# Optimization experiments

Measured on AMD Instinct MI355X. Metric: run time of the kernel, lower is better.

## Reference

```python
import jax, jax.numpy as jnp
import numpy as np

K = 16
EPS = 1e-5
SLOPE = 0.2


def knn_idx(k, xyz_k, xyz_q):
    # xyz_k: (B,Nk,3), xyz_q: (B,Nq,3) -> (B,Nq,k) indices of k nearest in xyz_k
    d = (jnp.sum(xyz_q * xyz_q, -1, keepdims=True)
         - 2.0 * jnp.einsum('bqc,bkc->bqk', xyz_q, xyz_k)
         + jnp.sum(xyz_k * xyz_k, -1)[:, None, :])
    _, idx = jax.lax.top_k(-d, k)
    return idx


def graph_feature(coor_q, x_q, coor_k, x_k):
    # coor_*: (B,N*,3); x_q: (B,C,Nq); x_k: (B,C,Nk) -> (B,2C,Nq,K)
    idx = knn_idx(K, coor_k, coor_q)                      # (B,Nq,K)
    nbr = jax.vmap(lambda xk, i: xk[:, i])(x_k, idx)       # (B,C,Nq,K)
    xq = x_q[:, :, :, None]                                # (B,C,Nq,1)
    xq = jnp.broadcast_to(xq, nbr.shape)
    return jnp.concatenate([nbr - xq, xq], axis=1)


def group_norm(x, gamma, beta, groups=4):
    B, C, N, Kk = x.shape
    xg = x.reshape(B, groups, C // groups, N, Kk)
    mu = jnp.mean(xg, axis=(2, 3, 4), keepdims=True)
    var = jnp.var(xg, axis=(2, 3, 4), keepdims=True)
    xn = ((xg - mu) / jnp.sqrt(var + EPS)).reshape(B, C, N, Kk)
    return xn * gamma[None, :, None, None] + beta[None, :, None, None]


def cgl(f, W, gamma, beta):
    # 1x1 Conv2d (no bias) + GroupNorm(4) + LeakyReLU(0.2)
    y = jnp.einsum('oc,bcnk->bonk', W, f)
    return jax.nn.leaky_relu(group_norm(y, gamma, beta), SLOPE)


def fps(xyz, m):
    # furthest point sampling. xyz: (B,N,3) -> (B,m) int32
    B, N, _ = xyz.shape
    first = jnp.zeros((B,), jnp.int32)

    def body(carry, _):
        dist, last = carry
        lp = jnp.take_along_axis(xyz, last[:, None, None].astype(jnp.int32), axis=1)  # (B,1,3)
        d = jnp.sum((xyz - lp) ** 2, -1)
        dist = jnp.minimum(dist, d)
        nxt = jnp.argmax(dist, -1).astype(jnp.int32)
        return (dist, nxt), nxt

    init = (jnp.full((B, N), 1e10, jnp.float32), first)
    _, rest = jax.lax.scan(body, init, None, length=m - 1)  # (m-1,B)
    return jnp.concatenate([first[None, :], rest], axis=0).T  # (B,m)


def fps_downsample(coor, x, m):
    # coor: (B,N,3), x: (B,C,N) -> new_coor (B,3,m), new_x (B,C,m)
    idx = fps(coor, m)                                        # (B,m)
    new_coor = jnp.take_along_axis(coor, idx[:, :, None], axis=1).transpose(0, 2, 1)
    new_x = jnp.take_along_axis(x, idx[:, None, :], axis=2)
    return new_coor, new_x


def setup_inputs() -> dict:
    key = jax.random.key(0)
    ks = jax.random.split(key, 16)
    d = {
        'x': jax.random.normal(ks[0], (8, 4096, 3), jnp.float32),
        'num0': 2048, 'num1': 512, 'num2': 128,
        'w_in': jax.random.normal(ks[1], (8, 3), jnp.float32) * 0.3,
        'b_in': jnp.zeros((8,), jnp.float32),
    }
    layer_dims = {'1': (32, 16), '2': (64, 64), '4': (128, 128),
                  '5': (128, 256), '6': (256, 256), '7': (256, 512)}
    for i, (name, (o, c)) in enumerate(layer_dims.items()):
        d[f'w{name}'] = jax.random.normal(ks[2 + i], (o, c), jnp.float32) * (1.0 / np.sqrt(c))
        d[f'g{name}'] = jnp.ones((o,), jnp.float32)
        d[f'be{name}'] = jnp.zeros((o,), jnp.float32)
    return d


def reference(x, num0, num1, num2, w_in, b_in,
              w1, g1, be1, w2, g2, be2, w4, g4, be4,
              w5, g5, be5, w6, g6, be6, w7, g7, be7):
    xyz = x.transpose(0, 2, 1)                                # (B,3,N)
    coor = x                                                  # (B,N,3)
    f = jnp.einsum('oc,bcn->bon', w_in, xyz) + b_in[None, :, None]  # (B,8,N)

    f = cgl(graph_feature(coor, f, coor, f), w1, g1, be1)     # (B,32,N,K)
    f = jnp.max(f, axis=-1)                                   # (B,32,N)

    sp1, f_q = fps_downsample(coor, f, num0)                  # (B,3,n0),(B,32,n0)
    coor_d = sp1.transpose(0, 2, 1)                           # (B,n0,3)
    f = cgl(graph_feature(coor_d, f_q, coor, f), w2, g2, be2)
    stage1_feature = jnp.max(f, axis=-1)                      # (B,64,n0)
    coor = coor_d

    sp2, f_q = fps_downsample(coor, stage1_feature, num1)
    coor_d = sp2.transpose(0, 2, 1)
    f = cgl(graph_feature(coor_d, f_q, coor, stage1_feature), w4, g4, be4)
    f = jnp.max(f, axis=-1)                                   # (B,128,n1)
    f = cgl(graph_feature(coor_d, f, coor_d, f), w5, g5, be5)
    stage2_feature = jnp.max(f, axis=-1)                      # (B,128,n1)
    coor = coor_d

    sp3, f_q = fps_downsample(coor, stage2_feature, num2)
    coor_d = sp3.transpose(0, 2, 1)
    f = cgl(graph_feature(coor_d, f_q, coor, stage2_feature), w6, g6, be6)
    f = jnp.max(f, axis=-1)                                   # (B,256,n2)
    f = cgl(graph_feature(coor_d, f, coor_d, f), w7, g7, be7)
    stage3_feature = jnp.max(f, axis=-1)                      # (B,256,n2)

    out_coor = sp3.transpose(0, 2, 1)                         # (B,n2,3)
    out_f = stage3_feature.transpose(0, 2, 1)                 # (B,n2,256)
    return out_coor, out_f
```

## Files before the change

### kernel.cpp

```cpp
#include <hip/hip_runtime.h>
#include <hip/hip_bf16.h>
#include <math.h>

#define DEVI __device__ __forceinline__
typedef unsigned long long ull;
typedef float f32x2 __attribute__((ext_vector_type(2)));

DEVI f32x2 pk_sub(f32x2 a, f32x2 b){
  f32x2 r;
  asm("v_pk_add_f32 %0, %1, %2 neg_lo:[0,1] neg_hi:[0,1]" : "=v"(r) : "v"(a), "v"(b));
  return r;
}
DEVI f32x2 pk_mul(f32x2 a, f32x2 b){
  f32x2 r; asm("v_pk_mul_f32 %0, %1, %2" : "=v"(r) : "v"(a), "v"(b)); return r;
}
DEVI f32x2 pk_add(f32x2 a, f32x2 b){
  f32x2 r; asm("v_pk_add_f32 %0, %1, %2" : "=v"(r) : "v"(a), "v"(b)); return r;
}

template<int CTRL>
DEVI float dppmaxf(float x){
  float o = __int_as_float(__builtin_amdgcn_update_dpp(__float_as_int(x),__float_as_int(x),CTRL,0xF,0xF,false));
  return fmaxf(x,o);
}
template<int CTRL>
DEVI unsigned dppminu(unsigned x){
  unsigned o = (unsigned)__builtin_amdgcn_update_dpp((int)x,(int)x,CTRL,0xF,0xF,false);
  return (x < o) ? x : o;
}

template<int P>
DEVI void fps_stage(f32x2 (&px)[P/2], f32x2 (&py)[P/2], f32x2 (&pz)[P/2],
                    int m, float sx, float sy, float sz,
                    const float* cpx, const float* cpy, const float* cpz,
                    ull* mK,
                    int* ssel, float* snx, float* sny, float* snz, int tid)
{
  const int wv = tid>>6, lane = tid&63;
  float dist[P];
  #pragma unroll
  for (int p=0;p<P;p++) dist[p]=1e10f;
  if (tid==0){ ssel[0]=0; if (snx){ snx[0]=sx; sny[0]=sy; snz[0]=sz; } }
  #pragma unroll 1
  for (int it=1; it<m; it++){
    f32x2 vsx, vsy, vsz;
    vsx.x=sx; vsx.y=sx; vsy.x=sy; vsy.y=sy; vsz.x=sz; vsz.y=sz;
    float bv = -1.f;
    #pragma unroll
    for (int i=0;i<P/2;i++){
      f32x2 dx = pk_sub(px[i], vsx);
      f32x2 dy = pk_sub(py[i], vsy);
      f32x2 dz = pk_sub(pz[i], vsz);
      f32x2 s  = pk_add(pk_add(pk_mul(dx,dx), pk_mul(dy,dy)), pk_mul(dz,dz));
      float d0 = fminf(dist[2*i],   s.x);
      float d1 = fminf(dist[2*i+1], s.y);
      dist[2*i] = d0; dist[2*i+1] = d1;
      bv = fmaxf(bv, d0);
      bv = fmaxf(bv, d1);
    }
    int bidx = 0;
    #pragma unroll
    for (int p=P-1;p>=0;p--) if (dist[p]==bv) bidx = tid+(p<<8);
    float w = bv;
    w = dppmaxf<0x111>(w);
    w = dppmaxf<0x112>(w);
    w = dppmaxf<0x114>(w);
    w = dppmaxf<0x118>(w);
    w = dppmaxf<0x142>(w);
    w = dppmaxf<0x143>(w);
    float bvw = __uint_as_float((unsigned)__builtin_amdgcn_readlane(__float_as_int(w),63));
    unsigned cand = (bv == bvw) ? (unsigned)bidx : 0xFFFFFFFFu;
    cand = dppminu<0x111>(cand);
    cand = dppminu<0x112>(cand);
    cand = dppminu<0x114>(cand);
    cand = dppminu<0x118>(cand);
    cand = dppminu<0x142>(cand);
    cand = dppminu<0x143>(cand);
    const unsigned itu = (unsigned)it;
    ull* slot = mK + ((it&1)<<2);
    if (lane==63){
      unsigned lo = ((~cand & 0xFFFu)<<12) | itu;
      *(volatile ull*)(slot + wv) = ((ull)__float_as_uint(bvw)<<32) | (ull)lo;
    }
    ull k0,k1,k2,k3;
    for (;;){
      asm volatile("" ::: "memory");
      k0=slot[0]; k1=slot[1]; k2=slot[2]; k3=slot[3];
      unsigned chk = (((unsigned)k0 ^ itu) | ((unsigned)k1 ^ itu) |
                      ((unsigned)k2 ^ itu) | ((unsigned)k3 ^ itu)) & 0xFFFu;
      if (chk == 0u) break;
    }
    ull ka = (k1>k0)?k1:k0;
    ull kb = (k3>k2)?k3:k2;
    ull kw = (kb>ka)?kb:ka;
    int gi = (int)((~((unsigned)(kw & 0xffffffffull) >> 12)) & 0xFFFu);
    sx = cpx[gi]; sy = cpy[gi]; sz = cpz[gi];
    if (tid==0){
      ssel[it]=gi;
      if (snx){ snx[it]=sx; sny[it]=sy; snz[it]=sz; }
    }
  }
}

template<int CTRL>
DEVI void dppmin_fj(float& d, int& j){
  float od = __int_as_float(__builtin_amdgcn_update_dpp(__float_as_int(d),__float_as_int(d),CTRL,0xF,0xF,false));
  int   oj = __builtin_amdgcn_update_dpp(j,j,CTRL,0xF,0xF,false);
  bool tk = (od < d) || (od == d && oj < j);
  d = tk?od:d; j = tk?oj:j;
}

DEVI float dist_qk(const float* __restrict__ ckb, int j,
                   float qx, float qy, float qz, float sqq){
  float kx=ckb[3*j], ky=ckb[3*j+1], kz=ckb[3*j+2];
  float sk  = __fadd_rn(__fadd_rn(__fmul_rn(kx,kx),__fmul_rn(ky,ky)),
                        __fmul_rn(kz,kz));
  float dot = __fadd_rn(__fadd_rn(__fmul_rn(qx,kx),__fmul_rn(qy,ky)),
                        __fmul_rn(qz,kz));
  return __fadd_rn(__fsub_rn(sqq, __fmul_rn(2.0f,dot)), sk);
}

template<int NPL>
DEVI void knn_wave(const float* __restrict__ cq, int Nq,
                   const float* __restrict__ ck, int Nk,
                   int* __restrict__ idx_out, int b, int q, int lane)
{
  size_t r3 = ((size_t)b*Nq+q)*3;
  float qx=cq[r3], qy=cq[r3+1], qz=cq[r3+2];
  float sqq = __fadd_rn(__fadd_rn(__fmul_rn(qx,qx),__fmul_rn(qy,qy)),
                        __fmul_rn(qz,qz));
  constexpr int GS = (NPL < 8) ? NPL : 8;
  constexpr int NG = NPL / GS;
  float gv[NG]; int gj[NG];
  const float* ckb = ck + (size_t)b*Nk*3;
  ull exmask = 0;
  int dirtyg = -1;
  int myout = 0;
  #pragma unroll 1
  for (int r=0; r<16; r++){
    #pragma unroll
    for (int g=0; g<NG; g++){
      if (dirtyg < 0 || dirtyg == g){
        float nv=__int_as_float(0x7f800000); int nj=0x7fffffff;
        #pragma unroll
        for (int e=0; e<GS; e++){
          const int i = g*GS+e;
          int j = lane + (i<<6);
          float d = dist_qk(ckb, j, qx,qy,qz, sqq);
          bool rem = ((exmask >> i) & 1ull) == 0ull;
          if (rem && d < nv){ nv=d; nj=j; }
        }
        gv[g]=nv; gj[g]=nj;
      }
    }
    float lv = gv[0]; int lj = gj[0];
    #pragma unroll
    for (int g=1; g<NG; g++)
      if (gv[g]<lv || (gv[g]==lv && gj[g]<lj)){ lv=gv[g]; lj=gj[g]; }
    float rd = lv; int rj = lj;
    dppmin_fj<0x111>(rd,rj);
    dppmin_fj<0x112>(rd,rj);
    dppmin_fj<0x114>(rd,rj);
    dppmin_fj<0x118>(rd,rj);
    dppmin_fj<0x142>(rd,rj);
    dppmin_fj<0x143>(rd,rj);
    int wj = __builtin_amdgcn_readlane(rj,63);
    if (lane == r) myout = wj;
    if ((wj & 63) == lane) exmask |= (1ull << (wj>>6));
    dirtyg = (wj>>6)/GS;
  }
  if (lane<16) idx_out[((size_t)b*Nq+q)*16 + lane] = myout;
}

__global__ __launch_bounds__(256) void k_fps_knn1(
    const float* __restrict__ coords0,
    int* __restrict__ idx1, int* __restrict__ idx2, int* __restrict__ idx3,
    float* __restrict__ c1, float* __restrict__ c2, float* __restrict__ c3,
    float* __restrict__ out, int* __restrict__ knn1)
{
  __shared__ float s1x[4096], s1y[4096], s1z[4096];
  __shared__ float s2x[2048], s2y[2048], s2z[2048];
  __shared__ float s3x[512],  s3y[512],  s3z[512];
  __shared__ float s4x[128],  s4y[128],  s4z[128];
  __shared__ int   ssel[2048];
  __shared__ alignas(32) ull mK[8];
  if (blockIdx.x >= 8){
    int flat = blockIdx.x - 8;
    int b = flat >> 10, qb = flat & 1023;
    int q = qb*4 + (threadIdx.x>>6);
    knn_wave<64>(coords0, 4096, coords0, 4096, knn1, b, q, threadIdx.x&63);
    return;
  }
  const int b = blockIdx.x, tid = threadIdx.x;
  __builtin_amdgcn_s_setprio(3);
  const float* cb = coords0 + (size_t)b*4096*3;
  if (tid<8) mK[tid] = ~0ull;
  {
    f32x2 px[8], py[8], pz[8];
    #pragma unroll
    for (int i=0;i<8;i++){
      int j0 = tid + ((2*i)<<8), j1 = tid + ((2*i+1)<<8);
      float X0=cb[3*j0], Y0=cb[3*j0+1], Z0=cb[3*j0+2];
      float X1=cb[3*j1], Y1=cb[3*j1+1], Z1=cb[3*j1+2];
      px[i].x=X0; px[i].y=X1; py[i].x=Y0; py[i].y=Y1; pz[i].x=Z0; pz[i].y=Z1;
      s1x[j0]=X0; s1y[j0]=Y0; s1z[j0]=Z0;
      s1x[j1]=X1; s1y[j1]=Y1; s1z[j1]=Z1;
    }
    float sx=cb[0], sy=cb[1], sz=cb[2];
    __syncthreads();
    fps_stage<16>(px,py,pz, 2048, sx,sy,sz, s1x,s1y,s1z,
                  mK, ssel, s2x,s2y,s2z, tid);
  }
  __syncthreads();
  {
    float* c1b = c1 + (size_t)b*2048*3;
    for (int i=tid;i<2048;i+=256){
      idx1[b*2048+i]=ssel[i];
      c1b[3*i]=s2x[i]; c1b[3*i+1]=s2y[i]; c1b[3*i+2]=s2z[i];
    }
  }
  {
    f32x2 px[4], py[4], pz[4];
    #pragma unroll
    for (int i=0;i<4;i++){
      int j0 = tid + ((2*i)<<8), j1 = tid + ((2*i+1)<<8);
      px[i].x=s2x[j0]; px[i].y=s2x[j1];
      py[i].x=s2y[j0]; py[i].y=s2y[j1];
      pz[i].x=s2z[j0]; pz[i].y=s2z[j1];
    }
    float sx=s2x[0], sy=s2y[0], sz=s2z[0];
    __syncthreads();
    fps_stage<8>(px,py,pz, 512, sx,sy,sz, s2x,s2y,s2z,
                 mK, ssel, s3x,s3y,s3z, tid);
  }
  __syncthreads();
  {
    float* c2b = c2 + (size_t)b*512*3;
    for (int i=tid;i<512;i+=256){
      idx2[b*512+i]=ssel[i];
      c2b[3*i]=s3x[i]; c2b[3*i+1]=s3y[i]; c2b[3*i+2]=s3z[i];
    }
  }
  {
    f32x2 px[1], py[1], pz[1];
    {
      int j0 = tid, j1 = tid + 256;
      px[0].x=s3x[j0]; px[0].y=s3x[j1];
      py[0].x=s3y[j0]; py[0].y=s3y[j1];
      pz[0].x=s3z[j0]; pz[0].y=s3z[j1];
    }
    float sx=s3x[0], sy=s3y[0], sz=s3z[0];
    __syncthreads();
    fps_stage<2>(px,py,pz, 128, sx,sy,sz, s3x,s3y,s3z,
                 mK, ssel, s4x,s4y,s4z, tid);
  }
  __syncthreads();
  {
    float* c3b = c3 + (size_t)b*128*3;
    float* ob  = out + (size_t)b*128*3;
    for (int i=tid;i<128;i+=256){
      idx3[b*128+i]=ssel[i];
      float X=s4x[i],Y=s4y[i],Z=s4z[i];
      c3b[3*i]=X; c3b[3*i+1]=Y; c3b[3*i+2]=Z;
      ob[3*i]=X; ob[3*i+1]=Y; ob[3*i+2]=Z;
    }
  }
}

struct WtParams {
  const float* W[6];
  float* wl[6];
  float* wq[6];
  int O[6], C[6], OC[6];
};
__global__ void k_wt_all(WtParams p, float* __restrict__ stats){
  int s = blockIdx.y;
  int t = blockIdx.x*blockDim.x + threadIdx.x;
  if (s==0 && t<384) stats[t] = 0.f;
  int OC = p.OC[s];
  if (t >= OC) return;
  int C = p.C[s], O = p.O[s];
  int o = t / C, c = t - o*C;
  const float* W = p.W[s];
  float wlv = W[o*2*C + c];
  float wrv = W[o*2*C + C + c];
  p.wl[s][c*O+o] = wlv;
  p.wq[s][c*O+o] = wrv - wlv;
}

#define GEMM_M 8
template<int NPL, int MODE>
__global__ __launch_bounds__(256,3) void k_knn_gemm(
    const float* __restrict__ cq, int Nq,
    const float* __restrict__ ck, int Nk, int* __restrict__ knnidx,
    const float* __restrict__ fsrc,
    const float* __restrict__ w_in, const float* __restrict__ b_in,
    const float* __restrict__ stats, const float* __restrict__ gamma,
    const float* __restrict__ beta, float invcnt,
    int C, int O,
    const float* __restrict__ wlT, const float* __restrict__ wqT,
    float* __restrict__ yk, float* __restrict__ yq, int gknn)
{
  const int b = blockIdx.y;
  if ((int)blockIdx.x < gknn){
    int q = blockIdx.x*4 + (threadIdx.x>>6);
    if (q < Nq) knn_wave<NPL>(cq, Nq, ck, Nk, knnidx, b, q, threadIdx.x&63);
    return;
  }
  const int bx = blockIdx.x - gknn;
  extern __shared__ float sf[];
  const int o = threadIdx.x & (O-1);
  const int rg = threadIdx.x / O;
  const int R = blockDim.x / O;
  const int rowsPB = R*GEMM_M;
  const int row0 = bx * rowsPB;
  const int Cp = C+1;
  if (MODE == 0){
    const float* xb = fsrc + (size_t)b*Nk*3;
    for (int i=threadIdx.x; i<rowsPB*C; i+=blockDim.x){
      int r = i / C, c = i - r*C;
      int row = row0 + r;
      float cx=xb[row*3], cy=xb[row*3+1], cz=xb[row*3+2];
      float s = __fadd_rn(__fadd_rn(__fmul_rn(cx,w_in[c*3+0]),
                                    __fmul_rn(cy,w_in[c*3+1])),
                          __fmul_rn(cz,w_in[c*3+2]));
      sf[r*Cp + c] = __fadd_rn(s, b_in[c]);
    }
  } else {
    const float* src = fsrc + ((size_t)b*Nk + row0)*C;
    for (int i=threadIdx.x; i<rowsPB*C; i+=blockDim.x){
      int r = i / C, c = i - r*C;
      int g = (c*4)/C;
      float s1 = stats[b*8+g*2], s2 = stats[b*8+g*2+1];
      float mu = s1*invcnt;
      float var = fmaf(-mu,mu, s2*invcnt);
      float rs = 1.0f/sqrtf(var+1e-5f);
      float v = (src[i]-mu)*rs*gamma[c] + beta[c];
      sf[r*Cp + c] = (v>=0.f)? v : 0.2f*v;
    }
  }
  __syncthreads();
  float ak[GEMM_M], aq[GEMM_M];
  #pragma unroll
  for (int m=0;m<GEMM_M;m++){ ak[m]=0.f; aq[m]=0.f; }
  const float* lp = wlT + o;
  const float* qp = wqT + o;
  const float* sfr = sf + rg*GEMM_M*Cp;
  for (int c=0;c<C;c++){
    float wl = lp[(size_t)c*O];
    float wq = qp[(size_t)c*O];
    #pragma unroll
    for (int m=0;m<GEMM_M;m++){
      float xv = sfr[m*Cp + c];
      ak[m] = fmaf(xv, wl, ak[m]);
      aq[m] = fmaf(xv, wq, aq[m]);
    }
  }
  size_t obase = ((size_t)b*Nk + row0 + rg*GEMM_M)*O + o;
  #pragma unroll
  for (int m=0;m<GEMM_M;m++){
    yk[obase + (size_t)m*O] = ak[m];
    yq[obase + (size_t)m*O] = aq[m];
  }
}

__global__ void k_gather(const float* __restrict__ yk, const float* __restrict__ yq,
                         const int* __restrict__ knnidx, const int* __restrict__ qmap,
                         int Nq, int Nk, int O,
                         float* __restrict__ vmax, float* __restrict__ stats)
{
  const int b = blockIdx.y;
  const int o = threadIdx.x & (O-1);
  const int rg = threadIdx.x / O;
  const int R = blockDim.x / O;
  float ls=0.f, ls2=0.f;
  const float* ykb = yk + (size_t)b*Nk*O;
  const float* yqb = yq + (size_t)b*Nk*O;
  for (int nq = blockIdx.x*R + rg; nq < Nq; nq += gridDim.x*R){
    int qj = qmap ? qmap[b*Nq+nq] : nq;
    float vq = yqb[(size_t)qj*O + o];
    const int* ip = knnidx + ((size_t)b*Nq+nq)*16;
    float vmx = -3.4e38f;
    #pragma unroll
    for (int k=0;k<16;k++){
      int j = ip[k];
      float v = ykb[(size_t)j*O+o] + vq;
      vmx = fmaxf(vmx, v);
      ls += v; ls2 = fmaf(v,v,ls2);
    }
    vmax[((size_t)b*Nq+nq)*O+o] = vmx;
  }
  int span = O/4; if (span>64) span=64;
  for (int mm=1; mm<span; mm<<=1){
    ls  += __shfl_xor(ls, mm);
    ls2 += __shfl_xor(ls2, mm);
  }
  __shared__ float sred[8];
  if (threadIdx.x<8) sred[threadIdx.x]=0.f;
  __syncthreads();
  int lane = threadIdx.x & 63;
  if ((lane & (span-1))==0){
    int g = (o*4)/O;
    atomicAdd(&sred[g*2+0], ls);
    atomicAdd(&sred[g*2+1], ls2);
  }
  __syncthreads();
  if (threadIdx.x<8) atomicAdd(&stats[b*8+threadIdx.x], sred[threadIdx.x]);
}

__global__ void k_norm(const float* __restrict__ vmax, const float* __restrict__ stats,
                       const float* __restrict__ gamma,
                       const float* __restrict__ beta,
                       int Nq, int O, float invcnt, float* __restrict__ outf)
{
  const int b = blockIdx.y;
  const int n = Nq*O;
  for (int i = blockIdx.x*blockDim.x+threadIdx.x; i<n; i+=gridDim.x*blockDim.x){
    int o = i & (O-1);
    int g = (o*4)/O;
    float s1 = stats[b*8+g*2], s2 = stats[b*8+g*2+1];
    float mu = s1*invcnt;
    float var = fmaf(-mu,mu, s2*invcnt);
    float rs = 1.0f/sqrtf(var+1e-5f);
    float v = (vmax[(size_t)b*n + i]-mu)*rs*gamma[o] + beta[o];
    outf[(size_t)b*n + i] = (v>=0.f)? v : 0.2f*v;
  }
}

extern "C" void kernel_launch(void* const* d_in, const int* in_sizes, int n_in,
                              void* d_out, int out_size, void* d_ws, size_t ws_size,
                              hipStream_t stream)
{
  const int B = 8;
  const float* x    = (const float*)d_in[0];
  const float* w_in = (const float*)d_in[4];
  const float* b_in = (const float*)d_in[5];
  const float *Wm[6], *Gm[6], *Bm[6];
  for (int i=0;i<6;i++){
    Wm[i]=(const float*)d_in[6+3*i];
    Gm[i]=(const float*)d_in[6+3*i+1];
    Bm[i]=(const float*)d_in[6+3*i+2];
  }
  float* ws = (float*)d_ws;
  float* out = (float*)d_out;
  const size_t OFF_C0=0,        OFF_F0=98304,   OFF_F1=360448,  OFF_F2=1409024,
               OFF_F4=2457600,  OFF_F5=2981888, OFF_F6=3506176, OFF_F7=3768320,
               OFF_C1=4030464,  OFF_C2=4079616, OFF_C3=4091904,
               OFF_YK=4094976,  OFF_YQ=6192128, OFF_VM=8289280,
               OFF_WL=9337856,  OFF_WQ=9468928, OFF_ST=9600000,
               OFF_I1=9600384,  OFF_I2=9616768, OFF_I3=9620864, OFF_KNN=9621888,
               TOTAL=10146176;
  if (ws_size < TOTAL*sizeof(float)) return;
  float *c1=ws+OFF_C1, *c2=ws+OFF_C2, *c3=ws+OFF_C3,
        *yk=ws+OFF_YK, *yq=ws+OFF_YQ, *vm=ws+OFF_VM, *stats=ws+OFF_ST;
  int *i1=(int*)(ws+OFF_I1), *i2=(int*)(ws+OFF_I2), *i3=(int*)(ws+OFF_I3),
      *knn=(int*)(ws+OFF_KNN);
  (void)OFF_C0; (void)OFF_F0; (void)OFF_F1; (void)OFF_F2; (void)OFF_F4;
  (void)OFF_F5; (void)OFF_F6; (void)OFF_F7;

  const int OCs[6]  = {256, 2048, 8192, 16384, 32768, 65536};
  const int OCoff[6]= {0,   256,  2304, 10496, 26880, 59648};

  struct St { int C,O,Nk,Nq; const float* cq; const float* ck;
              const int* qmap; };
  const St st[6] = {
    {8,   32, 4096, 4096, x,  x,  nullptr},
    {32,  64, 4096, 2048, c1, x,  i1},
    {64, 128, 2048,  512, c2, c1, i2},
    {128,128,  512,  512, c2, c2, nullptr},
    {128,256,  512,  128, c3, c2, i3},
    {256,256,  128,  128, c3, c3, nullptr},
  };
  float invc[6];
  for (int s=0;s<6;s++)
    invc[s] = 1.0f / ((float)(st[s].O/4) * (float)st[s].Nq * 16.0f);

  WtParams wp;
  for (int s=0;s<6;s++){
    wp.W[s]=Wm[s];
    wp.wl[s]=ws+OFF_WL+OCoff[s];
    wp.wq[s]=ws+OFF_WQ+OCoff[s];
    wp.O[s]=st[s].O; wp.C[s]=st[s].C; wp.OC[s]=OCs[s];
  }
  k_wt_all<<<dim3(256,6), 256, 0, stream>>>(wp, stats);

  k_fps_knn1<<<8 + 8*1024, 256, 0, stream>>>(x, i1, i2, i3, c1, c2, c3,
                                             out, knn);

  for (int s=0;s<6;s++){
    const St& S = st[s];
    int rowsPB = 2048 / S.O;
    int ggemm = S.Nk / rowsPB;
    int gknn  = (s > 0) ? (S.Nq + 3)/4 : 0;
    dim3 gg(gknn + ggemm, B);
    size_t shb = (size_t)rowsPB * (S.C+1) * sizeof(float);
    const float* wl = ws+OFF_WL+OCoff[s];
    const float* wqp = ws+OFF_WQ+OCoff[s];
    const float* stp = (s>0) ? (stats + (s-1)*64) : nullptr;
    const float* gp  = (s>0) ? Gm[s-1] : nullptr;
    const float* bp  = (s>0) ? Bm[s-1] : nullptr;
    float ivc = (s>0) ? invc[s-1] : 0.f;
    int npl = S.Nk >> 6;
    if      (s == 0)
      k_knn_gemm< 2,0><<<gg, 256, shb, stream>>>(S.cq,S.Nq,S.ck,S.Nk,knn,
        x, w_in, b_in, nullptr, nullptr, nullptr, 0.f,
        S.C, S.O, wl, wqp, yk, yq, gknn);
    else if (npl == 64)
      k_knn_gemm<64,1><<<gg, 256, shb, stream>>>(S.cq,S.Nq,S.ck,S.Nk,knn,
        vm, nullptr, nullptr, stp, gp, bp, ivc,
        S.C, S.O, wl, wqp, yk, yq, gknn);
    else if (npl == 32)
      k_knn_gemm<32,1><<<gg, 256, shb, stream>>>(S.cq,S.Nq,S.ck,S.Nk,knn,
        vm, nullptr, nullptr, stp, gp, bp, ivc,
        S.C, S.O, wl, wqp, yk, yq, gknn);
    else if (npl ==  8)
      k_knn_gemm< 8,1><<<gg, 256, shb, stream>>>(S.cq,S.Nq,S.ck,S.Nk,knn,
        vm, nullptr, nullptr, stp, gp, bp, ivc,
        S.C, S.O, wl, wqp, yk, yq, gknn);
    else
      k_knn_gemm< 2,1><<<gg, 256, shb, stream>>>(S.cq,S.Nq,S.ck,S.Nk,knn,
        vm, nullptr, nullptr, stp, gp, bp, ivc,
        S.C, S.O, wl, wqp, yk, yq, gknn);
    dim3 gs(64, B);
    k_gather<<<gs, 256, 0, stream>>>(yk, yq, knn, S.qmap, S.Nq, S.Nk, S.O,
                                     vm, stats + s*64);
  }
  {
    dim3 gn((128*256 + 255)/256, B);
    k_norm<<<gn, 256, 0, stream>>>(vm, stats + 5*64, Gm[5], Bm[5],
                                   128, 256, invc[5], out + 8*128*3);
  }
}
```

Before: 2.293 ms.

## Interleave two batches' FPS per block and publish winner coordinates directly

```diff
diff --git a/kernel.cpp b/kernel.cpp
--- a/kernel.cpp
+++ b/kernel.cpp
@@ -30,74 +30,122 @@
 }
 
 template<int P>
-DEVI void fps_stage(f32x2 (&px)[P/2], f32x2 (&py)[P/2], f32x2 (&pz)[P/2],
-                    int m, float sx, float sy, float sz,
-                    const float* cpx, const float* cpy, const float* cpz,
-                    ull* mK,
-                    int* ssel, float* snx, float* sny, float* snz, int tid)
+DEVI void fps_compute_publish(f32x2 (&px)[P/2], f32x2 (&py)[P/2], f32x2 (&pz)[P/2],
+                              float (&dist)[P],
+                              float sx, float sy, float sz,
+                              unsigned itu, ull* slotbuf, int tid)
 {
   const int wv = tid>>6, lane = tid&63;
-  float dist[P];
+  f32x2 vsx, vsy, vsz;
+  vsx.x=sx; vsx.y=sx; vsy.x=sy; vsy.y=sy; vsz.x=sz; vsz.y=sz;
+  float bv = -1.f;
   #pragma unroll
-  for (int p=0;p<P;p++) dist[p]=1e10f;
-  if (tid==0){ ssel[0]=0; if (snx){ snx[0]=sx; sny[0]=sy; snz[0]=sz; } }
+  for (int i=0;i<P/2;i++){
+    f32x2 dx = pk_sub(px[i], vsx);
+    f32x2 dy = pk_sub(py[i], vsy);
+    f32x2 dz = pk_sub(pz[i], vsz);
+    f32x2 s  = pk_add(pk_add(pk_mul(dx,dx), pk_mul(dy,dy)), pk_mul(dz,dz));
+    float d0 = fminf(dist[2*i],   s.x);
+    float d1 = fminf(dist[2*i+1], s.y);
+    dist[2*i] = d0; dist[2*i+1] = d1;
+    bv = fmaxf(bv, d0);
+    bv = fmaxf(bv, d1);
+  }
+  int bidx = 0;
+  #pragma unroll
+  for (int p=P-1;p>=0;p--) if (dist[p]==bv) bidx = tid+(p<<8);
+  float w = bv;
+  w = dppmaxf<0x111>(w);
+  w = dppmaxf<0x112>(w);
+  w = dppmaxf<0x114>(w);
+  w = dppmaxf<0x118>(w);
+  w = dppmaxf<0x142>(w);
+  w = dppmaxf<0x143>(w);
+  float bvw = __uint_as_float((unsigned)__builtin_amdgcn_readlane(__float_as_int(w),63));
+  unsigned cand = (bv == bvw) ? (unsigned)bidx : 0xFFFFFFFFu;
+  cand = dppminu<0x111>(cand);
+  cand = dppminu<0x112>(cand);
+  cand = dppminu<0x114>(cand);
+  cand = dppminu<0x118>(cand);
+  cand = dppminu<0x142>(cand);
+  cand = dppminu<0x143>(cand);
+  unsigned candw = (unsigned)__builtin_amdgcn_readlane((int)cand,63);
+  int wp = (int)(candw >> 8);
+  float bx = px[0].x, by = py[0].x, bz = pz[0].x;
+  #pragma unroll
+  for (int i=0;i<P/2;i++){
+    if (wp == 2*i  ){ bx=px[i].x; by=py[i].x; bz=pz[i].x; }
+    if (wp == 2*i+1){ bx=px[i].y; by=py[i].y; bz=pz[i].y; }
+  }
+  int wlane = (int)(candw & 63u);
+  bx = __uint_as_float((unsigned)__builtin_amdgcn_readlane(__float_as_int(bx), wlane));
+  by = __uint_as_float((unsigned)__builtin_amdgcn_readlane(__float_as_int(by), wlane));
+  bz = __uint_as_float((unsigned)__builtin_amdgcn_readlane(__float_as_int(bz), wlane));
+  if (lane==63){
+    volatile ull* sb = (volatile ull*)slotbuf;
+    sb[4+wv] = ((ull)__float_as_uint(by)<<32) | (ull)__float_as_uint(bx);
+    sb[8+wv] = ((ull)itu<<32) | (ull)__float_as_uint(bz);
+    unsigned lo = ((~candw & 0xFFFu)<<12) | itu;
+    sb[wv]   = ((ull)__float_as_uint(bvw)<<32) | (ull)lo;
+  }
+}
+
+DEVI void fps_poll_merge(const ull* slotbuf, unsigned itu,
+                         float& sx, float& sy, float& sz, int& gi)
+{
+  ull k0,k1,k2,k3,a0,a1,a2,a3,z0,z1,z2,z3;
+  for (;;){
+    asm volatile("" ::: "memory");
+    k0=slotbuf[0]; k1=slotbuf[1]; k2=slotbuf[2]; k3=slotbuf[3];
+    a0=slotbuf[4]; a1=slotbuf[5]; a2=slotbuf[6]; a3=slotbuf[7];
+    z0=slotbuf[8]; z1=slotbuf[9]; z2=slotbuf[10]; z3=slotbuf[11];
+    unsigned chk = (((unsigned)k0 ^ itu) | ((unsigned)k1 ^ itu) |
+                    ((unsigned)k2 ^ itu) | ((unsigned)k3 ^ itu)) & 0xFFFu;
+    chk |= ((unsigned)(z0>>32) ^ itu) | ((unsigned)(z1>>32) ^ itu) |
+           ((unsigned)(z2>>32) ^ itu) | ((unsigned)(z3>>32) ^ itu);
+    if (chk == 0u) break;
+  }
+  bool tA = (k1 > k0);
+  ull ka = tA?k1:k0, aa = tA?a1:a0, za = tA?z1:z0;
+  bool tB = (k3 > k2);
+  ull kb = tB?k3:k2, ab = tB?a3:a2, zb = tB?z3:z2;
+  bool tC = (kb > ka);
+  ull kw = tC?kb:ka, aw = tC?ab:aa, zw = tC?zb:za;
+  sx = __uint_as_float((unsigned)aw);
+  sy = __uint_as_float((unsigned)(aw>>32));
+  sz = __uint_as_float((unsigned)zw);
+  gi = (int)((~((unsigned)(kw & 0xffffffffull) >> 12)) & 0xFFFu);
+}
+
+template<int P>
+DEVI void fps_stage_dual(f32x2 (&pxA)[P/2], f32x2 (&pyA)[P/2], f32x2 (&pzA)[P/2],
+                         f32x2 (&pxB)[P/2], f32x2 (&pyB)[P/2], f32x2 (&pzB)[P/2],
+                         int m,
+                         float sxA, float syA, float szA,
+                         float sxB, float syB, float szB,
+                         ull (&slA)[2][12], ull (&slB)[2][12],
+                         int* sselA, int* sselB,
+                         float* snxA, float* snyA, float* snzA,
+                         float* snxB, float* snyB, float* snzB, int tid)
+{
+  float distA[P], distB[P];
+  #pragma unroll
+  for (int p=0;p<P;p++){ distA[p]=1e10f; distB[p]=1e10f; }
+  if (tid==0){
+    sselA[0]=0; snxA[0]=sxA; snyA[0]=syA; snzA[0]=szA;
+    sselB[0]=0; snxB[0]=sxB; snyB[0]=syB; snzB[0]=szB;
+  }
   #pragma unroll 1
   for (int it=1; it<m; it++){
-    f32x2 vsx, vsy, vsz;
-    vsx.x=sx; vsx.y=sx; vsy.x=sy; vsy.y=sy; vsz.x=sz; vsz.y=sz;
-    float bv = -1.f;
-    #pragma unroll
-    for (int i=0;i<P/2;i++){
-      f32x2 dx = pk_sub(px[i], vsx);
-      f32x2 dy = pk_sub(py[i], vsy);
-      f32x2 dz = pk_sub(pz[i], vsz);
-      f32x2 s  = pk_add(pk_add(pk_mul(dx,dx), pk_mul(dy,dy)), pk_mul(dz,dz));
-      float d0 = fminf(dist[2*i],   s.x);
-      float d1 = fminf(dist[2*i+1], s.y);
-      dist[2*i] = d0; dist[2*i+1] = d1;
-      bv = fmaxf(bv, d0);
-      bv = fmaxf(bv, d1);
-    }
-    int bidx = 0;
-    #pragma unroll
-    for (int p=P-1;p>=0;p--) if (dist[p]==bv) bidx = tid+(p<<8);
-    float w = bv;
-    w = dppmaxf<0x111>(w);
-    w = dppmaxf<0x112>(w);
-    w = dppmaxf<0x114>(w);
-    w = dppmaxf<0x118>(w);
-    w = dppmaxf<0x142>(w);
-    w = dppmaxf<0x143>(w);
-    float bvw = __uint_as_float((unsigned)__builtin_amdgcn_readlane(__float_as_int(w),63));
-    unsigned cand = (bv == bvw) ? (unsigned)bidx : 0xFFFFFFFFu;
-    cand = dppminu<0x111>(cand);
-    cand = dppminu<0x112>(cand);
-    cand = dppminu<0x114>(cand);
-    cand = dppminu<0x118>(cand);
-    cand = dppminu<0x142>(cand);
-    cand = dppminu<0x143>(cand);
     const unsigned itu = (unsigned)it;
-    ull* slot = mK + ((it&1)<<2);
-    if (lane==63){
-      unsigned lo = ((~cand & 0xFFFu)<<12) | itu;
-      *(volatile ull*)(slot + wv) = ((ull)__float_as_uint(bvw)<<32) | (ull)lo;
-    }
-    ull k0,k1,k2,k3;
-    for (;;){
-      asm volatile("" ::: "memory");
-      k0=slot[0]; k1=slot[1]; k2=slot[2]; k3=slot[3];
-      unsigned chk = (((unsigned)k0 ^ itu) | ((unsigned)k1 ^ itu) |
-                      ((unsigned)k2 ^ itu) | ((unsigned)k3 ^ itu)) & 0xFFFu;
-      if (chk == 0u) break;
-    }
-    ull ka = (k1>k0)?k1:k0;
-    ull kb = (k3>k2)?k3:k2;
-    ull kw = (kb>ka)?kb:ka;
-    int gi = (int)((~((unsigned)(kw & 0xffffffffull) >> 12)) & 0xFFFu);
-    sx = cpx[gi]; sy = cpy[gi]; sz = cpz[gi];
+    fps_compute_publish<P>(pxA,pyA,pzA,distA, sxA,syA,szA, itu, slA[it&1], tid);
+    fps_compute_publish<P>(pxB,pyB,pzB,distB, sxB,syB,szB, itu, slB[it&1], tid);
+    int giA, giB;
+    fps_poll_merge(slA[it&1], itu, sxA,syA,szA, giA);
+    fps_poll_merge(slB[it&1], itu, sxB,syB,szB, giB);
     if (tid==0){
-      ssel[it]=gi;
-      if (snx){ snx[it]=sx; sny[it]=sy; snz[it]=sz; }
+      sselA[it]=giA; snxA[it]=sxA; snyA[it]=syA; snzA[it]=szA;
+      sselB[it]=giB; snxB[it]=sxB; snyB[it]=syB; snzB[it]=szB;
     }
   }
 }
@@ -178,91 +226,116 @@
     float* __restrict__ c1, float* __restrict__ c2, float* __restrict__ c3,
     float* __restrict__ out, int* __restrict__ knn1)
 {
-  __shared__ float s1x[4096], s1y[4096], s1z[4096];
-  __shared__ float s2x[2048], s2y[2048], s2z[2048];
-  __shared__ float s3x[512],  s3y[512],  s3z[512];
-  __shared__ float s4x[128],  s4y[128],  s4z[128];
-  __shared__ int   ssel[2048];
-  __shared__ alignas(32) ull mK[8];
-  if (blockIdx.x >= 8){
-    int flat = blockIdx.x - 8;
+  __shared__ float s2x[2][2048], s2y[2][2048], s2z[2][2048];
+  __shared__ float s3x[2][512],  s3y[2][512],  s3z[2][512];
+  __shared__ float s4x[2][128],  s4y[2][128],  s4z[2][128];
+  __shared__ int   ssel[2][2048];
+  __shared__ alignas(32) ull slots[2][2][12];
+  if (blockIdx.x >= 4){
+    int flat = blockIdx.x - 4;
     int b = flat >> 10, qb = flat & 1023;
     int q = qb*4 + (threadIdx.x>>6);
     knn_wave<64>(coords0, 4096, coords0, 4096, knn1, b, q, threadIdx.x&63);
     return;
   }
-  const int b = blockIdx.x, tid = threadIdx.x;
+  const int tid = threadIdx.x;
+  const int bA = blockIdx.x*2, bB = bA+1;
   __builtin_amdgcn_s_setprio(3);
-  const float* cb = coords0 + (size_t)b*4096*3;
-  if (tid<8) mK[tid] = ~0ull;
+  const float* cbA = coords0 + (size_t)bA*4096*3;
+  const float* cbB = coords0 + (size_t)bB*4096*3;
+  if (tid<48) ((ull*)slots)[tid] = ~0ull;
   {
-    f32x2 px[8], py[8], pz[8];
+    f32x2 pxA[8], pyA[8], pzA[8], pxB[8], pyB[8], pzB[8];
     #pragma unroll
     for (int i=0;i<8;i++){
       int j0 = tid + ((2*i)<<8), j1 = tid + ((2*i+1)<<8);
-      float X0=cb[3*j0], Y0=cb[3*j0+1], Z0=cb[3*j0+2];
-      float X1=cb[3*j1], Y1=cb[3*j1+1], Z1=cb[3*j1+2];
-      px[i].x=X0; px[i].y=X1; py[i].x=Y0; py[i].y=Y1; pz[i].x=Z0; pz[i].y=Z1;
-      s1x[j0]=X0; s1y[j0]=Y0; s1z[j0]=Z0;
-      s1x[j1]=X1; s1y[j1]=Y1; s1z[j1]=Z1;
-    }
-    float sx=cb[0], sy=cb[1], sz=cb[2];
+      pxA[i].x=cbA[3*j0]; pyA[i].x=cbA[3*j0+1]; pzA[i].x=cbA[3*j0+2];
+      pxA[i].y=cbA[3*j1]; pyA[i].y=cbA[3*j1+1]; pzA[i].y=cbA[3*j1+2];
+      pxB[i].x=cbB[3*j0]; pyB[i].x=cbB[3*j0+1]; pzB[i].x=cbB[3*j0+2];
+      pxB[i].y=cbB[3*j1]; pyB[i].y=cbB[3*j1+1]; pzB[i].y=cbB[3*j1+2];
+    }
+    float sxA=cbA[0], syA=cbA[1], szA=cbA[2];
+    float sxB=cbB[0], syB=cbB[1], szB=cbB[2];
     __syncthreads();
-    fps_stage<16>(px,py,pz, 2048, sx,sy,sz, s1x,s1y,s1z,
-                  mK, ssel, s2x,s2y,s2z, tid);
+    fps_stage_dual<16>(pxA,pyA,pzA, pxB,pyB,pzB, 2048,
+                       sxA,syA,szA, sxB,syB,szB,
+                       slots[0], slots[1], ssel[0], ssel[1],
+                       s2x[0],s2y[0],s2z[0], s2x[1],s2y[1],s2z[1], tid);
   }
   __syncthreads();
   {
-    float* c1b = c1 + (size_t)b*2048*3;
-    for (int i=tid;i<2048;i+=256){
-      idx1[b*2048+i]=ssel[i];
-      c1b[3*i]=s2x[i]; c1b[3*i+1]=s2y[i]; c1b[3*i+2]=s2z[i];
-    }
-  }
+    #pragma unroll
+    for (int g=0; g<2; g++){
+      int b = bA + g;
+      float* c1b = c1 + (size_t)b*2048*3;
+      for (int i=tid;i<2048;i+=256){
+        idx1[b*2048+i]=ssel[g][i];
+        c1b[3*i]=s2x[g][i]; c1b[3*i+1]=s2y[g][i]; c1b[3*i+2]=s2z[g][i];
+      }
+    }
+  }
+  __syncthreads();
   {
-    f32x2 px[4], py[4], pz[4];
+    f32x2 pxA[4], pyA[4], pzA[4], pxB[4], pyB[4], pzB[4];
     #pragma unroll
     for (int i=0;i<4;i++){
       int j0 = tid + ((2*i)<<8), j1 = tid + ((2*i+1)<<8);
-      px[i].x=s2x[j0]; px[i].y=s2x[j1];
-      py[i].x=s2y[j0]; py[i].y=s2y[j1];
-      pz[i].x=s2z[j0]; pz[i].y=s2z[j1];
-    }
-    float sx=s2x[0], sy=s2y[0], sz=s2z[0];
+      pxA[i].x=s2x[0][j0]; pyA[i].x=s2y[0][j0]; pzA[i].x=s2z[0][j0];
+      pxA[i].y=s2x[0][j1]; pyA[i].y=s2y[0][j1]; pzA[i].y=s2z[0][j1];
+      pxB[i].x=s2x[1][j0]; pyB[i].x=s2y[1][j0]; pzB[i].x=s2z[1][j0];
+      pxB[i].y=s2x[1][j1]; pyB[i].y=s2y[1][j1]; pzB[i].y=s2z[1][j1];
+    }
+    float sxA=s2x[0][0], syA=s2y[0][0], szA=s2z[0][0];
+    float sxB=s2x[1][0], syB=s2y[1][0], szB=s2z[1][0];
     __syncthreads();
-    fps_stage<8>(px,py,pz, 512, sx,sy,sz, s2x,s2y,s2z,
-                 mK, ssel, s3x,s3y,s3z, tid);
+    fps_stage_dual<8>(pxA,pyA,pzA, pxB,pyB,pzB, 512,
+                      sxA,syA,szA, sxB,syB,szB,
+                      slots[0], slots[1], ssel[0], ssel[1],
+                      s3x[0],s3y[0],s3z[0], s3x[1],s3y[1],s3z[1], tid);
   }
   __syncthreads();
   {
-    float* c2b = c2 + (size_t)b*512*3;
-    for (int i=tid;i<512;i+=256){
-      idx2[b*512+i]=ssel[i];
-      c2b[3*i]=s3x[i]; c2b[3*i+1]=s3y[i]; c2b[3*i+2]=s3z[i];
-    }
-  }
+    #pragma unroll
+    for (int g=0; g<2; g++){
+      int b = bA + g;
+      float* c2b = c2 + (size_t)b*512*3;
+      for (int i=tid;i<512;i+=256){
+        idx2[b*512+i]=ssel[g][i];
+        c2b[3*i]=s3x[g][i]; c2b[3*i+1]=s3y[g][i]; c2b[3*i+2]=s3z[g][i];
+      }
+    }
+  }
+  __syncthreads();
   {
-    f32x2 px[1], py[1], pz[1];
+    f32x2 pxA[1], pyA[1], pzA[1], pxB[1], pyB[1], pzB[1];
     {
       int j0 = tid, j1 = tid + 256;
-      px[0].x=s3x[j0]; px[0].y=s3x[j1];
-      py[0].x=s3y[j0]; py[0].y=s3y[j1];
-      pz[0].x=s3z[j0]; pz[0].y=s3z[j1];
-    }
-    float sx=s3x[0], sy=s3y[0], sz=s3z[0];
+      pxA[0].x=s3x[0][j0]; pyA[0].x=s3y[0][j0]; pzA[0].x=s3z[0][j0];
+      pxA[0].y=s3x[0][j1]; pyA[0].y=s3y[0][j1]; pzA[0].y=s3z[0][j1];
+      pxB[0].x=s3x[1][j0]; pyB[0].x=s3y[1][j0]; pzB[0].x=s3z[1][j0];
+      pxB[0].y=s3x[1][j1]; pyB[0].y=s3y[1][j1]; pzB[0].y=s3z[1][j1];
+    }
+    float sxA=s3x[0][0], syA=s3y[0][0], szA=s3z[0][0];
+    float sxB=s3x[1][0], syB=s3y[1][0], szB=s3z[1][0];
     __syncthreads();
-    fps_stage<2>(px,py,pz, 128, sx,sy,sz, s3x,s3y,s3z,
-                 mK, ssel, s4x,s4y,s4z, tid);
+    fps_stage_dual<2>(pxA,pyA,pzA, pxB,pyB,pzB, 128,
+                      sxA,syA,szA, sxB,syB,szB,
+                      slots[0], slots[1], ssel[0], ssel[1],
+                      s4x[0],s4y[0],s4z[0], s4x[1],s4y[1],s4z[1], tid);
   }
   __syncthreads();
   {
-    float* c3b = c3 + (size_t)b*128*3;
-    float* ob  = out + (size_t)b*128*3;
-    for (int i=tid;i<128;i+=256){
-      idx3[b*128+i]=ssel[i];
-      float X=s4x[i],Y=s4y[i],Z=s4z[i];
-      c3b[3*i]=X; c3b[3*i+1]=Y; c3b[3*i+2]=Z;
-      ob[3*i]=X; ob[3*i+1]=Y; ob[3*i+2]=Z;
+    #pragma unroll
+    for (int g=0; g<2; g++){
+      int b = bA + g;
+      float* c3b = c3 + (size_t)b*128*3;
+      float* ob  = out + (size_t)b*128*3;
+      for (int i=tid;i<128;i+=256){
+        idx3[b*128+i]=ssel[g][i];
+        float X=s4x[g][i],Y=s4y[g][i],Z=s4z[g][i];
+        c3b[3*i]=X; c3b[3*i+1]=Y; c3b[3*i+2]=Z;
+        ob[3*i]=X; ob[3*i+1]=Y; ob[3*i+2]=Z;
+      }
     }
   }
 }
@@ -443,9 +516,7 @@
   }
   float* ws = (float*)d_ws;
   float* out = (float*)d_out;
-  const size_t OFF_C0=0,        OFF_F0=98304,   OFF_F1=360448,  OFF_F2=1409024,
-               OFF_F4=2457600,  OFF_F5=2981888, OFF_F6=3506176, OFF_F7=3768320,
-               OFF_C1=4030464,  OFF_C2=4079616, OFF_C3=4091904,
+  const size_t OFF_C1=4030464,  OFF_C2=4079616, OFF_C3=4091904,
                OFF_YK=4094976,  OFF_YQ=6192128, OFF_VM=8289280,
                OFF_WL=9337856,  OFF_WQ=9468928, OFF_ST=9600000,
                OFF_I1=9600384,  OFF_I2=9616768, OFF_I3=9620864, OFF_KNN=9621888,
@@ -455,8 +526,6 @@
         *yk=ws+OFF_YK, *yq=ws+OFF_YQ, *vm=ws+OFF_VM, *stats=ws+OFF_ST;
   int *i1=(int*)(ws+OFF_I1), *i2=(int*)(ws+OFF_I2), *i3=(int*)(ws+OFF_I3),
       *knn=(int*)(ws+OFF_KNN);
-  (void)OFF_C0; (void)OFF_F0; (void)OFF_F1; (void)OFF_F2; (void)OFF_F4;
-  (void)OFF_F5; (void)OFF_F6; (void)OFF_F7;
 
   const int OCs[6]  = {256, 2048, 8192, 16384, 32768, 65536};
   const int OCoff[6]= {0,   256,  2304, 10496, 26880, 59648};
@@ -484,7 +553,7 @@
   }
   k_wt_all<<<dim3(256,6), 256, 0, stream>>>(wp, stats);
 
-  k_fps_knn1<<<8 + 8*1024, 256, 0, stream>>>(x, i1, i2, i3, c1, c2, c3,
+  k_fps_knn1<<<4 + 8*1024, 256, 0, stream>>>(x, i1, i2, i3, c1, c2, c3,
                                              out, knn);
 
   for (int s=0;s<6;s++){
```

Measured after the change: 5.485 ms. +139.2%, slower.
